# Kernel optimization log

Measured on AMD Instinct MI355X. Metric: run time of the kernel, lower is better.

## Reference

```python
import jax, jax.numpy as jnp
import numpy as np

B, N, U = 8, 2048, 256
BN_EPS = 1e-3  # keras BatchNormalization default epsilon
ADJ_DENSITY = 0.008  # ~16 neighbors per node on average


def setup_inputs() -> dict:
    key = jax.random.key(0)
    ks = jax.random.split(key, 16)
    s = 0.05  # weight scale ('random_normal' init is small-stddev in keras)
    x = jax.random.normal(ks[0], (B, N, U), jnp.float32)
    # sparse binary adjacency stored dense (per-sample SpMM pattern)
    adj = (jax.random.uniform(ks[1], (B, N, N)) < ADJ_DENSITY).astype(jnp.float32)
    nodal_mask = jnp.ones((B, N), jnp.float32)
    return {
        'x': x, 'adj': adj, 'nodal_mask': nodal_mask,
        'W_lin': jax.random.normal(ks[2], (U, U)) * s, 'b_lin': jnp.zeros((U,)),
        'Wq_mp': jax.random.normal(ks[3], (3, U, U)) * s, 'bq_mp': jnp.zeros((3, U)),
        'Wk_mp': jax.random.normal(ks[4], (3, U, U)) * s, 'bk_mp': jnp.zeros((3, U)),
        'Wv_mp': jax.random.normal(ks[5], (3, U, U)) * s, 'bv_mp': jnp.zeros((3, U)),
        'Wk_att': jax.random.normal(ks[6], (U, U)) * s,
        'Wv_att': jax.random.normal(ks[7], (U, U)) * s,
        'Wq_att': jax.random.normal(ks[8], (U, U)) * s,
        'Wo_att': jax.random.normal(ks[9], (U, U)) * s,
        'bn_gamma': jnp.ones((U,)), 'bn_beta': jnp.zeros((U,)),
        'bn_mean': jnp.zeros((U,)), 'bn_var': jnp.ones((U,)),
        'W_proj': jax.random.normal(ks[10], (U, U)) * s, 'b_proj': jnp.zeros((U,)),
        'W_res': jax.random.normal(ks[11], (U, U)) * s, 'b_res': jnp.zeros((U,)),
    }


def _dympn(x, adj, Ws, bs, mask):
    # 3 message-passing layers, each applied K_l=2 times (inference value)
    for i in range(3):
        for _ in range(2):
            xn = jnp.einsum('bmn,bnd->bmd', adj, x)  # batched SpMM (graph_conv mode)
            x = jax.nn.silu(jnp.einsum('bmd,de->bme', xn, Ws[i]) + bs[i])
    return x * mask[:, :, None]


def reference(x, adj, nodal_mask, W_lin, b_lin, Wq_mp, bq_mp, Wk_mp, bk_mp,
              Wv_mp, bv_mp, Wk_att, Wv_att, Wq_att, Wo_att,
              bn_gamma, bn_beta, bn_mean, bn_var, W_proj, b_proj, W_res, b_res):
    initial_x = x
    adj = jax.lax.stop_gradient(adj)
    h = jnp.einsum('bnd,de->bne', x, W_lin) + b_lin
    q = _dympn(h, adj, Wq_mp, bq_mp, nodal_mask)
    k = _dympn(h, adj, Wk_mp, bk_mp, nodal_mask)
    v = _dympn(h, adj, Wv_mp, bv_mp, nodal_mask)
    # linear attention
    m = nodal_mask[:, :, None]
    pk = jax.nn.silu(jnp.einsum('bnd,de->bne', k, Wk_att) * m)
    pv = jnp.einsum('bnd,de->bne', v, Wv_att) * m
    pq = jnp.einsum('bnd,de->bne', q, Wq_att)
    kv = jnp.einsum('bnd,bne->bde', pk, pv)       # [B,U,U]
    attn = jnp.einsum('bnd,bde->bne', pq, kv)
    attn = jnp.einsum('bnd,de->bne', attn, Wo_att)
    # batch norm (inference: moving stats) over last axis
    y = attn + initial_x
    y = bn_gamma * (y - bn_mean) * jax.lax.rsqrt(bn_var + BN_EPS) + bn_beta
    out = jax.nn.silu(jnp.einsum('bnd,de->bne', y, W_proj) + b_proj)
    out = out + jnp.einsum('bnd,de->bne', initial_x, W_res) + b_res
    out = out * nodal_mask[:, :, None]
    return out
```

## Files before the change

### kernel.cpp

```cpp
#include <hip/hip_runtime.h>
#include <stdint.h>

#define NB 8
#define NN 2048
#define NU 256
#define CAP 64
#define BNEPS 0.001f
#define GSTR ((size_t)(NN * NU + 256))

typedef __attribute__((ext_vector_type(8))) short short8;
typedef __attribute__((ext_vector_type(4))) float floatx4;
typedef unsigned short u16;
typedef unsigned int u32;

__device__ __forceinline__ float bf2f(u16 u) {
  union { u32 i; float f; } c; c.i = ((u32)u) << 16; return c.f;
}
__device__ __forceinline__ u16 f2bf(float f) {
  union { float f; u32 i; } c; c.f = f;
  return (u16)((c.i + 0x7fffu + ((c.i >> 16) & 1u)) >> 16);
}
__device__ __forceinline__ void splitbf(float a, u16& h, u16& l) {
  h = f2bf(a);
  l = f2bf(a - bf2f(h));
}

enum : unsigned {
  F_BIAS = 2u, F_SILU = 4u, F_MASKPRE = 8u, F_MASKPOST = 16u,
  F_ADDX = 32u, F_BN = 64u, F_ADDT = 128u, F_BPERMAT = 512u,
  F_TPLANES = 1024u, F_OUTHL = 2048u, F_GSTRIDE = 8192u
};

#define TP_MAT 524288
#define TP_LO  4194304
#define MSZ ((size_t)NN * NU)

struct WPtrs { const float* p[16]; };

__global__ __launch_bounds__(256) void prologue_k(
    WPtrs wp, u16* __restrict__ wdst,
    const float* __restrict__ x, u16* __restrict__ xdst, size_t xLo,
    const float* __restrict__ adj, int* __restrict__ cnt, int* __restrict__ idx,
    float* __restrict__ ga, float* __restrict__ gb)
{
  int bid = blockIdx.x;
  int tid = threadIdx.x;
  __shared__ int c0;
  if (bid < 512) {
    int gid = bid * 256 + tid;
    int mat = gid >> 13;
    int rem = gid & 8191;
    int kb = rem >> 10;
    int n = (rem >> 2) & 255;
    int slot = rem & 3;
    int qv = (slot - (n >> 1)) & 3;
    int k0 = kb * 32 + qv * 8;
    const float* W = wp.p[mat];
    u32 oh[4], ol[4];
#pragma unroll
    for (int t2 = 0; t2 < 4; t2++) {
      float f0 = W[(size_t)(k0 + 2 * t2) * 256 + n];
      float f1 = W[(size_t)(k0 + 2 * t2 + 1) * 256 + n];
      u16 h0, l0, h1, l1;
      splitbf(f0, h0, l0);
      splitbf(f1, h1, l1);
      oh[t2] = (u32)h0 | ((u32)h1 << 16);
      ol[t2] = (u32)l0 | ((u32)l1 << 16);
    }
    uint4 qh; qh.x = oh[0]; qh.y = oh[1]; qh.z = oh[2]; qh.w = oh[3];
    uint4 ql; ql.x = ol[0]; ql.y = ol[1]; ql.z = ol[2]; ql.w = ol[3];
    *(uint4*)(wdst + (size_t)gid * 8) = qh;
    *(uint4*)(wdst + 1048576 + (size_t)gid * 8) = ql;
  } else if (bid < 4608) {
    size_t i = ((size_t)(bid - 512) * 256 + tid) * 4;
    float4 v = *(const float4*)(x + i);
    u16 h0, l0, h1, l1, h2, l2, h3, l3;
    splitbf(v.x, h0, l0); splitbf(v.y, h1, l1);
    splitbf(v.z, h2, l2); splitbf(v.w, h3, l3);
    uint2 H; H.x = (u32)h0 | ((u32)h1 << 16); H.y = (u32)h2 | ((u32)h3 << 16);
    uint2 L; L.x = (u32)l0 | ((u32)l1 << 16); L.y = (u32)l2 | ((u32)l3 << 16);
    *(uint2*)(xdst + i) = H;
    *(uint2*)(xdst + xLo + i) = L;
  } else if (bid < 20992) {
    int row = bid - 4608;
    const float* base = adj + (size_t)row * NN;
    if (tid == 0) c0 = 0;
    __syncthreads();
#pragma unroll
    for (int j = 0; j < 8; j++) {
      int n = j * 256 + tid;
      if (base[n] != 0.f) {
        int p = atomicAdd(&c0, 1);
        if (p < CAP) idx[(size_t)row * CAP + p] = n;
      }
    }
    __syncthreads();
    int cc = (c0 < CAP ? c0 : CAP);
    for (int p = cc + tid; p < CAP; p += 256) idx[(size_t)row * CAP + p] = -1;
    if (tid == 0) cnt[row] = cc;
  } else {
    int g = bid - 20992;
    float* base = (g < 24 ? ga : gb) + (size_t)(g % 24) * GSTR;
    base[tid] = 0.f;
  }
}

template <unsigned F>
__device__ __forceinline__ void gemm_epi(
    floatx4 (&acc)[2][2], int b, int bm, int w, int m16, int q,
    const float* __restrict__ bias, const float* __restrict__ mask,
    const float* __restrict__ xf32,
    const float* __restrict__ gma, const float* __restrict__ bta,
    const float* __restrict__ bmu, const float* __restrict__ bvr,
    const float* __restrict__ addt, void* __restrict__ outp, size_t oLo)
{
#pragma unroll
  for (int mt = 0; mt < 2; mt++) {
    if (F & F_TPLANES) {
      u16* oh = (u16*)outp + (size_t)b * TP_MAT;
      u16* ol = oh + TP_LO;
      int gr0 = bm + mt * 16 + q * 4;
#pragma unroll
      for (int nt = 0; nt < 2; nt++) {
        int col = w * 32 + nt * 16 + m16;
        u16 hh[4], ll[4];
#pragma unroll
        for (int r = 0; r < 4; r++) {
          float t2 = acc[mt][nt][r];
          float mv = mask[b * NN + gr0 + r];
          if (F & F_MASKPRE) t2 *= mv;
          if (F & F_SILU) t2 = t2 / (1.f + __expf(-t2));
          if (F & F_MASKPOST) t2 *= mv;
          splitbf(t2, hh[r], ll[r]);
        }
        uint2 H2, L2v;
        H2.x = (u32)hh[0] | ((u32)hh[1] << 16);
        H2.y = (u32)hh[2] | ((u32)hh[3] << 16);
        L2v.x = (u32)ll[0] | ((u32)ll[1] << 16);
        L2v.y = (u32)ll[2] | ((u32)ll[3] << 16);
        *(uint2*)(oh + (size_t)col * 2048 + gr0) = H2;
        *(uint2*)(ol + (size_t)col * 2048 + gr0) = L2v;
      }
    } else {
#pragma unroll
      for (int r = 0; r < 4; r++) {
        int gr = bm + mt * 16 + q * 4 + r;
        float mval = 1.f;
        if (F & (F_MASKPRE | F_MASKPOST)) mval = mask[b * NN + gr];
#pragma unroll
        for (int nt = 0; nt < 2; nt++) {
          int col = w * 32 + nt * 16 + m16;
          float t2 = acc[mt][nt][r];
          if (F & F_BIAS) t2 += bias[col];
          if (F & F_MASKPRE) t2 *= mval;
          if (F & F_SILU) t2 = t2 / (1.f + __expf(-t2));
          if (F & F_ADDX) t2 += xf32[((size_t)b * NN + gr) * NU + col];
          if (F & F_BN) t2 = gma[col] * (t2 - bmu[col]) * rsqrtf(bvr[col] + BNEPS) + bta[col];
          if (F & F_ADDT) t2 += addt[((size_t)b * NN + gr) * NU + col];
          if (F & F_MASKPOST) t2 *= mval;
          size_t o;
          if (F & F_GSTRIDE) o = (size_t)b * GSTR + (size_t)gr * NU + col;
          else o = ((size_t)b * NN + gr) * NU + col;
          if (F & F_OUTHL) {
            u16 h0, l0;
            splitbf(t2, h0, l0);
            ((u16*)outp)[o] = h0;
            ((u16*)outp)[o + oLo] = l0;
          } else {
            ((float*)outp)[o] = t2;
          }
        }
      }
    }
  }
}

template <int NG, unsigned SF, unsigned F0, unsigned F1, unsigned F2, bool DK = false>
__global__ __launch_bounds__(512, 4) void gemm_k(
    const u16* __restrict__ A0, const u16* __restrict__ A1, const u16* __restrict__ A2,
    size_t aLo,
    const u16* __restrict__ W0, const u16* __restrict__ W1, const u16* __restrict__ W2,
    size_t wLo,
    const float* __restrict__ b0, const float* __restrict__ b1, const float* __restrict__ b2,
    const float* __restrict__ mask,
    const float* __restrict__ xf32,
    const float* __restrict__ gma, const float* __restrict__ bta,
    const float* __restrict__ bmu, const float* __restrict__ bvr,
    const float* __restrict__ addt,
    void* __restrict__ o0, void* __restrict__ o1, void* __restrict__ o2,
    size_t oLo,
    const float* __restrict__ gsrc,
    const float* __restrict__ sb0, const float* __restrict__ sb1, const float* __restrict__ sb2,
    const int* __restrict__ ncnt, const int* __restrict__ nidx)
{
  const int tid = threadIdx.x;
  const int id = blockIdx.x;
  const int xcd = id & 7;
  const int t = id >> 3;
  const int chain = (NG == 1) ? 0 : (t >> 6);
  const int xt = (NG == 1) ? t : (t & 63);
  const int b = xcd;
  const int bm = xt * 32;

  __shared__ alignas(16) u16 Ah[32 * 264];
  __shared__ alignas(16) u16 Al[32 * 264];

  const u16* Wsel = (chain == 0) ? W0 : (chain == 1 ? W1 : W2);
  if (F0 & F_BPERMAT) Wsel = W0 + (size_t)b * 65536;
  const u16* Whi = Wsel;
  const u16* Wlo = Whi + wLo;

  const int lane = tid & 63;
  const int w = tid >> 6;

  if constexpr (SF != 0u) {
    const float* __restrict__ gm = gsrc + (size_t)(chain * 8 + b) * GSTR + 256;
    const float* sb = (chain == 0) ? sb0 : (chain == 1 ? sb1 : sb2);
    const int c = lane * 4;
    float4 bb = *(const float4*)(sb + c);
    const int r0 = w * 4;
    const int* ips[4];
    float4 av[4];
    int rowids[4];
    int maxc = 0;
#pragma unroll
    for (int i = 0; i < 4; i++) {
      rowids[i] = b * NN + bm + r0 + i;
      int cn = ncnt[rowids[i]];
      maxc = cn > maxc ? cn : maxc;
      ips[i] = nidx + (size_t)rowids[i] * CAP;
      av[i].x = av[i].y = av[i].z = av[i].w = 0.f;
    }
    maxc = (maxc + 3) & ~3;
#pragma unroll 1
    for (int e = 0; e < maxc; e += 4) {
#pragma unroll
      for (int i = 0; i < 4; i++) {
        int4 i4 = *(const int4*)(ips[i] + e);
        float4 v0 = *(const float4*)(gm + (ptrdiff_t)i4.x * 256 + c);
        float4 v1 = *(const float4*)(gm + (ptrdiff_t)i4.y * 256 + c);
        float4 v2 = *(const float4*)(gm + (ptrdiff_t)i4.z * 256 + c);
        float4 v3 = *(const float4*)(gm + (ptrdiff_t)i4.w * 256 + c);
        av[i].x += v0.x + v1.x + v2.x + v3.x;
        av[i].y += v0.y + v1.y + v2.y + v3.y;
        av[i].z += v0.z + v1.z + v2.z + v3.z;
        av[i].w += v0.w + v1.w + v2.w + v3.w;
      }
    }
#pragma unroll
    for (int i = 0; i < 4; i++) {
      float ov[4] = {av[i].x + bb.x, av[i].y + bb.y, av[i].z + bb.z, av[i].w + bb.w};
      float mv = (SF & F_MASKPOST) ? mask[rowids[i]] : 1.f;
      u16 hh[4], ll[4];
#pragma unroll
      for (int j = 0; j < 4; j++) {
        float t2 = ov[j];
        if (SF & F_SILU) t2 = t2 / (1.f + __expf(-t2));
        if (SF & F_MASKPOST) t2 *= mv;
        splitbf(t2, hh[j], ll[j]);
      }
      uint2 H; H.x = (u32)hh[0] | ((u32)hh[1] << 16); H.y = (u32)hh[2] | ((u32)hh[3] << 16);
      uint2 L; L.x = (u32)ll[0] | ((u32)ll[1] << 16); L.y = (u32)ll[2] | ((u32)ll[3] << 16);
      *(uint2*)&Ah[(r0 + i) * 264 + c] = H;
      *(uint2*)&Al[(r0 + i) * 264 + c] = L;
    }
  } else {
    const u16* Abase = (chain == 0) ? A0 : (chain == 1 ? A1 : A2);
    const u16* Ahp = Abase + (size_t)b * MSZ;
    const u16* Alp = Ahp + aLo;
    {
      int s = tid;
      int r = s >> 4;
      int c = (s & 15) << 4;
      size_t ao = (size_t)(bm + r) * 256 + c;
      *(uint4*)&Ah[r * 264 + c] = *(const uint4*)(Ahp + ao);
      *(uint4*)&Ah[r * 264 + c + 8] = *(const uint4*)(Ahp + ao + 8);
      *(uint4*)&Al[r * 264 + c] = *(const uint4*)(Alp + ao);
      *(uint4*)&Al[r * 264 + c + 8] = *(const uint4*)(Alp + ao + 8);
    }
  }
  __syncthreads();

  const int m16 = lane & 15;
  const int q = lane >> 4;

  floatx4 acc[2][2];
#pragma unroll
  for (int i = 0; i < 2; i++)
#pragma unroll
    for (int j = 0; j < 2; j++) acc[i][j] = (floatx4){0.f, 0.f, 0.f, 0.f};

#pragma unroll
  for (int kk = 0; kk < 8; kk++) {
    short8 bh[2], bl2[2];
#pragma unroll
    for (int nt = 0; nt < 2; nt++) {
      int n = w * 32 + nt * 16 + m16;
      size_t off = (size_t)kk * 8192 + (size_t)n * 32 + (size_t)(((q + (n >> 1)) & 3) * 8);
      bh[nt] = *(const short8*)(Whi + off);
      bl2[nt] = *(const short8*)(Wlo + off);
    }
#pragma unroll
    for (int mt = 0; mt < 2; mt++) {
      int row = mt * 16 + m16;
      short8 ah = *(const short8*)&Ah[row * 264 + kk * 32 + q * 8];
      short8 al2 = *(const short8*)&Al[row * 264 + kk * 32 + q * 8];
#pragma unroll
      for (int nt = 0; nt < 2; nt++) {
        acc[mt][nt] = __builtin_amdgcn_mfma_f32_16x16x32_bf16(ah, bh[nt], acc[mt][nt], 0, 0, 0);
        acc[mt][nt] = __builtin_amdgcn_mfma_f32_16x16x32_bf16(al2, bh[nt], acc[mt][nt], 0, 0, 0);
        acc[mt][nt] = __builtin_amdgcn_mfma_f32_16x16x32_bf16(ah, bl2[nt], acc[mt][nt], 0, 0, 0);
      }
    }
  }

  if constexpr (DK) {
#pragma unroll
    for (int mt = 0; mt < 2; mt++)
#pragma unroll
      for (int nt = 0; nt < 2; nt++) {
        int col = w * 32 + nt * 16 + m16;
        float bp = b1[col];
#pragma unroll
        for (int r = 0; r < 4; r++) {
          float t2 = acc[mt][nt][r] + bp;
          acc[mt][nt][r] = t2 / (1.f + __expf(-t2));
        }
      }
    __syncthreads();
    {
      const u16* Ahp = A1 + (size_t)b * MSZ;
      const u16* Alp = Ahp + aLo;
      int s = tid;
      int r = s >> 4;
      int c = (s & 15) << 4;
      size_t ao = (size_t)(bm + r) * 256 + c;
      *(uint4*)&Ah[r * 264 + c] = *(const uint4*)(Ahp + ao);
      *(uint4*)&Ah[r * 264 + c + 8] = *(const uint4*)(Ahp + ao + 8);
      *(uint4*)&Al[r * 264 + c] = *(const uint4*)(Alp + ao);
      *(uint4*)&Al[r * 264 + c + 8] = *(const uint4*)(Alp + ao + 8);
    }
    __syncthreads();
    const u16* W1h = W1;
    const u16* W1l = W1 + wLo;
#pragma unroll
    for (int kk = 0; kk < 8; kk++) {
      short8 bh[2], bl2[2];
#pragma unroll
      for (int nt = 0; nt < 2; nt++) {
        int n = w * 32 + nt * 16 + m16;
        size_t off = (size_t)kk * 8192 + (size_t)n * 32 + (size_t)(((q + (n >> 1)) & 3) * 8);
        bh[nt] = *(const short8*)(W1h + off);
        bl2[nt] = *(const short8*)(W1l + off);
      }
#pragma unroll
      for (int mt = 0; mt < 2; mt++) {
        int row = mt * 16 + m16;
        short8 ah = *(const short8*)&Ah[row * 264 + kk * 32 + q * 8];
        short8 al2 = *(const short8*)&Al[row * 264 + kk * 32 + q * 8];
#pragma unroll
        for (int nt = 0; nt < 2; nt++) {
          acc[mt][nt] = __builtin_amdgcn_mfma_f32_16x16x32_bf16(ah, bh[nt], acc[mt][nt], 0, 0, 0);
          acc[mt][nt] = __builtin_amdgcn_mfma_f32_16x16x32_bf16(al2, bh[nt], acc[mt][nt], 0, 0, 0);
          acc[mt][nt] = __builtin_amdgcn_mfma_f32_16x16x32_bf16(ah, bl2[nt], acc[mt][nt], 0, 0, 0);
        }
      }
    }
  }

  if (NG == 1 || chain == 0)
    gemm_epi<F0>(acc, b, bm, w, m16, q, b0, mask, xf32, gma, bta, bmu, bvr, addt, o0, oLo);
  else if (chain == 1)
    gemm_epi<F1>(acc, b, bm, w, m16, q, b1, mask, xf32, gma, bta, bmu, bvr, addt, o1, oLo);
  else
    gemm_epi<F2>(acc, b, bm, w, m16, q, b2, mask, xf32, gma, bta, bmu, bvr, addt, o2, oLo);
}

__global__ __launch_bounds__(256, 2) void kv_k(
    const u16* __restrict__ pkT, const u16* __restrict__ pvT, float* __restrict__ part)
{
  int et = blockIdx.x * 128;
  int dt = blockIdx.y * 128;
  int z = blockIdx.z;
  int b = z & 7;
  int p = z >> 3;
  int tid = threadIdx.x;
  int lane = tid & 63, w = tid >> 6;
  int m16 = lane & 15, q = lane >> 4;

  const u16* pkh = pkT + (size_t)b * TP_MAT;
  const u16* pkl = pkh + TP_LO;
  const u16* pvh = pvT + (size_t)b * TP_MAT;
  const u16* pvl = pvh + TP_LO;

  int d_base = dt + (w >> 1) * 64 + m16;
  int e_base = et + (w & 1) * 64 + m16;

  floatx4 acc[4][4];
#pragma unroll
  for (int i = 0; i < 4; i++)
#pragma unroll
    for (int j = 0; j < 4; j++) acc[i][j] = (floatx4){0.f, 0.f, 0.f, 0.f};

#pragma unroll
  for (int kt = 0; kt < 8; kt++) {
    int kc = p * 256 + kt * 32 + q * 8;
    short8 ah[4], al[4], bh[4], bl[4];
#pragma unroll
    for (int mt = 0; mt < 4; mt++) {
      size_t o = (size_t)(d_base + mt * 16) * 2048 + kc;
      ah[mt] = *(const short8*)(pkh + o);
      al[mt] = *(const short8*)(pkl + o);
    }
#pragma unroll
    for (int nt = 0; nt < 4; nt++) {
      size_t o = (size_t)(e_base + nt * 16) * 2048 + kc;
      bh[nt] = *(const short8*)(pvh + o);
      bl[nt] = *(const short8*)(pvl + o);
    }
#pragma unroll
    for (int mt = 0; mt < 4; mt++)
#pragma unroll
      for (int nt = 0; nt < 4; nt++) {
        acc[mt][nt] = __builtin_amdgcn_mfma_f32_16x16x32_bf16(ah[mt], bh[nt], acc[mt][nt], 0, 0, 0);
        acc[mt][nt] = __builtin_amdgcn_mfma_f32_16x16x32_bf16(al[mt], bh[nt], acc[mt][nt], 0, 0, 0);
        acc[mt][nt] = __builtin_amdgcn_mfma_f32_16x16x32_bf16(ah[mt], bl[nt], acc[mt][nt], 0, 0, 0);
      }
  }

#pragma unroll
  for (int mt = 0; mt < 4; mt++)
#pragma unroll
    for (int r = 0; r < 4; r++) {
      int d = dt + (w >> 1) * 64 + mt * 16 + q * 4 + r;
#pragma unroll
      for (int nt = 0; nt < 4; nt++) {
        int e = et + (w & 1) * 64 + nt * 16 + m16;
        part[(size_t)z * 65536 + (size_t)d * 256 + e] = acc[mt][nt][r];
      }
    }
}

__global__ __launch_bounds__(256) void kv_conv_k(const float* __restrict__ part, u16* __restrict__ dst)
{
  int gid = blockIdx.x * 256 + threadIdx.x;
  int b = gid >> 13;
  int rem = gid & 8191;
  int kb = rem >> 10;
  int e = (rem >> 2) & 255;
  int slot = rem & 3;
  int qv = (slot - (e >> 1)) & 3;
  int d0 = kb * 32 + qv * 8;
  const float* src = part + (size_t)b * 65536 + (size_t)d0 * 256 + e;
  u32 oh[4], ol[4];
#pragma unroll
  for (int t2 = 0; t2 < 4; t2++) {
    float s0 = 0.f, s1 = 0.f;
#pragma unroll
    for (int pp = 0; pp < 8; pp++) {
      const float* sp = src + (size_t)pp * 524288 + t2 * 512;
      s0 += sp[0];
      s1 += sp[256];
    }
    u16 h0, l0, h1, l1;
    splitbf(s0, h0, l0);
    splitbf(s1, h1, l1);
    oh[t2] = (u32)h0 | ((u32)h1 << 16);
    ol[t2] = (u32)l0 | ((u32)l1 << 16);
  }
  uint4 qh; qh.x = oh[0]; qh.y = oh[1]; qh.z = oh[2]; qh.w = oh[3];
  uint4 ql; ql.x = ol[0]; ql.y = ol[1]; ql.z = ol[2]; ql.w = ol[3];
  *(uint4*)(dst + (size_t)gid * 8) = qh;
  *(uint4*)(dst + 524288 + (size_t)gid * 8) = ql;
}

extern "C" void kernel_launch(void* const* d_in, const int* in_sizes, int n_in,
                              void* d_out, int out_size, void* d_ws, size_t ws_size,
                              hipStream_t stream)
{
  const float* x = (const float*)d_in[0];
  const float* adj = (const float*)d_in[1];
  const float* mask = (const float*)d_in[2];
  const float* W_lin = (const float*)d_in[3];
  const float* b_lin = (const float*)d_in[4];
  const float* Wq_mp = (const float*)d_in[5];
  const float* bq_mp = (const float*)d_in[6];
  const float* Wk_mp = (const float*)d_in[7];
  const float* bk_mp = (const float*)d_in[8];
  const float* Wv_mp = (const float*)d_in[9];
  const float* bv_mp = (const float*)d_in[10];
  const float* Wk_att = (const float*)d_in[11];
  const float* Wv_att = (const float*)d_in[12];
  const float* Wq_att = (const float*)d_in[13];
  const float* Wo_att = (const float*)d_in[14];
  const float* bn_gamma = (const float*)d_in[15];
  const float* bn_beta = (const float*)d_in[16];
  const float* bn_mean = (const float*)d_in[17];
  const float* bn_var = (const float*)d_in[18];
  const float* W_proj = (const float*)d_in[19];
  const float* b_proj = (const float*)d_in[20];
  const float* W_res = (const float*)d_in[21];
  const float* b_res = (const float*)d_in[22];

  char* ws = (char*)d_ws;
  int* CNT    = (int*)(ws + 0);
  int* IDX    = (int*)(ws + (1ull << 20));
  u16* WSZ    = (u16*)(ws + (5ull << 20));
  u16* KVS    = (u16*)(ws + (9ull << 20));
  float* KVP  = (float*)(ws + (11ull << 20));
  u16* XHL    = (u16*)(ws + (27ull << 20));
  u16* HHL    = (u16*)(ws + (43ull << 20));
  float* GA   = (float*)(ws + (59ull << 20));
  float* GB   = (float*)(ws + (110ull << 20));
  u16* PKT    = (u16*)(ws + (161ull << 20));
  u16* PVT    = (u16*)(ws + (177ull << 20));
  u16* ATT    = (u16*)(ws + (193ull << 20));
  u16* YHL    = (u16*)(ws + (209ull << 20));
  u16* PQHL   = (u16*)(ws + (225ull << 20));

  const size_t WLO = 1048576;
  const size_t KLO = 524288;
  const size_t A8  = 8 * MSZ;
  const unsigned FG = F_GSTRIDE;

  WPtrs wp;
  wp.p[0] = W_lin;
  wp.p[1] = Wq_mp; wp.p[2] = Wq_mp + 65536; wp.p[3] = Wq_mp + 131072;
  wp.p[4] = Wk_mp; wp.p[5] = Wk_mp + 65536; wp.p[6] = Wk_mp + 131072;
  wp.p[7] = Wv_mp; wp.p[8] = Wv_mp + 65536; wp.p[9] = Wv_mp + 131072;
  wp.p[10] = Wk_att; wp.p[11] = Wv_att; wp.p[12] = Wq_att; wp.p[13] = Wo_att;
  wp.p[14] = W_proj; wp.p[15] = W_res;
  prologue_k<<<21040, 256, 0, stream>>>(wp, WSZ, x, XHL, A8, adj, CNT, IDX, GA, GB);

  gemm_k<1, 0u, F_BIAS | F_OUTHL, 0u, 0u><<<512, 512, 0, stream>>>(
      XHL, XHL, XHL, A8, WSZ, WSZ, WSZ, WLO,
      b_lin, nullptr, nullptr, mask, nullptr,
      bn_gamma, bn_beta, bn_mean, bn_var, nullptr,
      HHL, nullptr, nullptr, A8,
      nullptr, nullptr, nullptr, nullptr, CNT, IDX);

  gemm_k<3, 0u, FG, FG, FG><<<1536, 512, 0, stream>>>(
      HHL, HHL, HHL, A8,
      WSZ + (size_t)1 * 65536, WSZ + (size_t)4 * 65536, WSZ + (size_t)7 * 65536, WLO,
      nullptr, nullptr, nullptr, mask, nullptr,
      bn_gamma, bn_beta, bn_mean, bn_var, nullptr,
      GA + 256, GA + 8 * GSTR + 256, GA + 16 * GSTR + 256, 0,
      nullptr, nullptr, nullptr, nullptr, CNT, IDX);

  for (int s = 1; s < 6; s++) {
    int iw = s >> 1;
    int ib = (s - 1) >> 1;
    float* Gin = (s & 1) ? GA : GB;
    float* Gout = (s & 1) ? GB : GA;
    gemm_k<3, F_BIAS | F_SILU, FG, FG, FG><<<1536, 512, 0, stream>>>(
        nullptr, nullptr, nullptr, 0,
        WSZ + (size_t)(1 + iw) * 65536, WSZ + (size_t)(4 + iw) * 65536,
        WSZ + (size_t)(7 + iw) * 65536, WLO,
        nullptr, nullptr, nullptr, mask, nullptr,
        bn_gamma, bn_beta, bn_mean, bn_var, nullptr,
        Gout + 256, Gout + 8 * GSTR + 256, Gout + 16 * GSTR + 256, 0,
        Gin, bq_mp + ib * 256, bk_mp + ib * 256, bv_mp + ib * 256, CNT, IDX);
  }

  gemm_k<3, F_BIAS | F_SILU | F_MASKPOST,
         F_OUTHL, F_SILU | F_MASKPRE | F_TPLANES, F_MASKPOST | F_TPLANES>
      <<<1536, 512, 0, stream>>>(
      nullptr, nullptr, nullptr, 0,
      WSZ + (size_t)12 * 65536, WSZ + (size_t)10 * 65536, WSZ + (size_t)11 * 65536, WLO,
      nullptr, nullptr, nullptr, mask, nullptr,
      bn_gamma, bn_beta, bn_mean, bn_var, nullptr,
      PQHL, PKT, PVT, A8,
      GB, bq_mp + 512, bk_mp + 512, bv_mp + 512, CNT, IDX);

  kv_k<<<dim3(2, 2, 64), 256, 0, stream>>>(PKT, PVT, KVP);
  kv_conv_k<<<256, 256, 0, stream>>>(KVP, KVS);

  gemm_k<1, 0u, F_BPERMAT | F_OUTHL, 0u, 0u><<<512, 512, 0, stream>>>(
      PQHL, PQHL, PQHL, A8, KVS, KVS, KVS, KLO,
      nullptr, nullptr, nullptr, mask, nullptr,
      bn_gamma, bn_beta, bn_mean, bn_var, nullptr,
      ATT, nullptr, nullptr, A8,
      nullptr, nullptr, nullptr, nullptr, CNT, IDX);

  gemm_k<1, 0u, F_ADDX | F_BN | F_OUTHL, 0u, 0u><<<512, 512, 0, stream>>>(
      ATT, ATT, ATT, A8,
      WSZ + (size_t)13 * 65536, nullptr, nullptr, WLO,
      nullptr, nullptr, nullptr, mask, x,
      bn_gamma, bn_beta, bn_mean, bn_var, nullptr,
      YHL, nullptr, nullptr, A8,
      nullptr, nullptr, nullptr, nullptr, CNT, IDX);

  gemm_k<1, 0u, F_BIAS | F_MASKPOST, 0u, 0u, true><<<512, 512, 0, stream>>>(
      YHL, XHL, YHL, A8,
      WSZ + (size_t)14 * 65536, WSZ + (size_t)15 * 65536, nullptr, WLO,
      b_res, b_proj, nullptr, mask, nullptr,
      bn_gamma, bn_beta, bn_mean, bn_var, nullptr,
      d_out, nullptr, nullptr, 0,
      nullptr, nullptr, nullptr, nullptr, CNT, IDX);

  (void)in_sizes; (void)n_in; (void)out_size; (void)ws_size;
}
```

Measured before the change: 754.4 us.

## Stage GSTRIDE epilogue through LDS with nontemporal stores, per-row gather bounds

```diff
diff --git a/kernel.cpp b/kernel.cpp
--- a/kernel.cpp
+++ b/kernel.cpp
@@ -158,9 +158,7 @@
           if (F & F_BN) t2 = gma[col] * (t2 - bmu[col]) * rsqrtf(bvr[col] + BNEPS) + bta[col];
           if (F & F_ADDT) t2 += addt[((size_t)b * NN + gr) * NU + col];
           if (F & F_MASKPOST) t2 *= mval;
-          size_t o;
-          if (F & F_GSTRIDE) o = (size_t)b * GSTR + (size_t)gr * NU + col;
-          else o = ((size_t)b * NN + gr) * NU + col;
+          size_t o = ((size_t)b * NN + gr) * NU + col;
           if (F & F_OUTHL) {
             u16 h0, l0;
             splitbf(t2, h0, l0);
@@ -176,7 +174,7 @@
 }
 
 template <int NG, unsigned SF, unsigned F0, unsigned F1, unsigned F2, bool DK = false>
-__global__ __launch_bounds__(512, 4) void gemm_k(
+__global__ __launch_bounds__(512, 8) void gemm_k(
     const u16* __restrict__ A0, const u16* __restrict__ A1, const u16* __restrict__ A2,
     size_t aLo,
     const u16* __restrict__ W0, const u16* __restrict__ W1, const u16* __restrict__ W2,
@@ -202,8 +200,9 @@
   const int b = xcd;
   const int bm = xt * 32;
 
-  __shared__ alignas(16) u16 Ah[32 * 264];
-  __shared__ alignas(16) u16 Al[32 * 264];
+  __shared__ alignas(16) u16 AB[2 * 32 * 264];
+  u16* const Ah = AB;
+  u16* const Al = AB + 32 * 264;
 
   const u16* Wsel = (chain == 0) ? W0 : (chain == 1 ? W1 : W2);
   if (F0 & F_BPERMAT) Wsel = W0 + (size_t)b * 65536;
@@ -219,32 +218,42 @@
     const int c = lane * 4;
     float4 bb = *(const float4*)(sb + c);
     const int r0 = w * 4;
+    int cnts[4];
     const int* ips[4];
     float4 av[4];
     int rowids[4];
-    int maxc = 0;
 #pragma unroll
     for (int i = 0; i < 4; i++) {
       rowids[i] = b * NN + bm + r0 + i;
-      int cn = ncnt[rowids[i]];
-      maxc = cn > maxc ? cn : maxc;
+      cnts[i] = ncnt[rowids[i]];
       ips[i] = nidx + (size_t)rowids[i] * CAP;
       av[i].x = av[i].y = av[i].z = av[i].w = 0.f;
     }
-    maxc = (maxc + 3) & ~3;
-#pragma unroll 1
-    for (int e = 0; e < maxc; e += 4) {
+    int maxc = cnts[0];
+    maxc = cnts[1] > maxc ? cnts[1] : maxc;
+    maxc = cnts[2] > maxc ? cnts[2] : maxc;
+    maxc = cnts[3] > maxc ? cnts[3] : maxc;
+    for (int e = 0; e + 4 <= maxc; e += 4) {
 #pragma unroll
       for (int i = 0; i < 4; i++) {
-        int4 i4 = *(const int4*)(ips[i] + e);
-        float4 v0 = *(const float4*)(gm + (ptrdiff_t)i4.x * 256 + c);
-        float4 v1 = *(const float4*)(gm + (ptrdiff_t)i4.y * 256 + c);
-        float4 v2 = *(const float4*)(gm + (ptrdiff_t)i4.z * 256 + c);
-        float4 v3 = *(const float4*)(gm + (ptrdiff_t)i4.w * 256 + c);
-        av[i].x += v0.x + v1.x + v2.x + v3.x;
-        av[i].y += v0.y + v1.y + v2.y + v3.y;
-        av[i].z += v0.z + v1.z + v2.z + v3.z;
-        av[i].w += v0.w + v1.w + v2.w + v3.w;
+        if (e + 4 <= cnts[i]) {
+          int4 i4 = *(const int4*)(ips[i] + e);
+          float4 v0 = *(const float4*)(gm + ((size_t)i4.x << 8) + c);
+          float4 v1 = *(const float4*)(gm + ((size_t)i4.y << 8) + c);
+          float4 v2 = *(const float4*)(gm + ((size_t)i4.z << 8) + c);
+          float4 v3 = *(const float4*)(gm + ((size_t)i4.w << 8) + c);
+          av[i].x += v0.x + v1.x + v2.x + v3.x;
+          av[i].y += v0.y + v1.y + v2.y + v3.y;
+          av[i].z += v0.z + v1.z + v2.z + v3.z;
+          av[i].w += v0.w + v1.w + v2.w + v3.w;
+        }
+      }
+    }
+#pragma unroll
+    for (int i = 0; i < 4; i++) {
+      for (int e = cnts[i] & ~3; e < cnts[i]; e++) {
+        float4 v = *(const float4*)(gm + ((size_t)ips[i][e] << 8) + c);
+        av[i].x += v.x; av[i].y += v.y; av[i].z += v.z; av[i].w += v.w;
       }
     }
 #pragma unroll
@@ -368,12 +377,36 @@
     }
   }
 
-  if (NG == 1 || chain == 0)
+  if constexpr ((F0 & F_GSTRIDE) != 0u) {
+    void* op = (NG == 1 || chain == 0) ? o0 : (chain == 1 ? o1 : o2);
+    __syncthreads();
+    float* Cf = (float*)AB;
+#pragma unroll
+    for (int mt = 0; mt < 2; mt++)
+#pragma unroll
+      for (int nt = 0; nt < 2; nt++) {
+        int col = w * 32 + nt * 16 + m16;
+#pragma unroll
+        for (int r = 0; r < 4; r++)
+          Cf[(mt * 16 + q * 4 + r) * 256 + col] = acc[mt][nt][r];
+      }
+    __syncthreads();
+    int r2 = tid >> 4;
+    int cs = (tid & 15) * 16;
+    float* dst = (float*)op + (size_t)b * GSTR + (size_t)(bm + r2) * 256 + cs;
+    const float* srcp = Cf + r2 * 256 + cs;
+#pragma unroll
+    for (int j = 0; j < 4; j++) {
+      floatx4 v4 = *(const floatx4*)(srcp + j * 4);
+      __builtin_nontemporal_store(v4, (floatx4*)(dst + j * 4));
+    }
+  } else if (NG == 1 || chain == 0) {
     gemm_epi<F0>(acc, b, bm, w, m16, q, b0, mask, xf32, gma, bta, bmu, bvr, addt, o0, oLo);
-  else if (chain == 1)
+  } else if (chain == 1) {
     gemm_epi<F1>(acc, b, bm, w, m16, q, b1, mask, xf32, gma, bta, bmu, bvr, addt, o1, oLo);
-  else
+  } else {
     gemm_epi<F2>(acc, b, bm, w, m16, q, b2, mask, xf32, gma, bta, bmu, bvr, addt, o2, oLo);
+  }
 }
 
 __global__ __launch_bounds__(256, 2) void kv_k(
```

New measurement: 991.3 us. +31.4%, slower.

## Stream SpMM neighbor gathers through per-wave LDS ring via global_load_lds

Applied to the files above, without the earlier changes.

```diff
diff --git a/kernel.cpp b/kernel.cpp
--- a/kernel.cpp
+++ b/kernel.cpp
@@ -8,6 +8,9 @@
 #define BNEPS 0.001f
 #define GSTR ((size_t)(NN * NU + 256))
 
+#define REG16 2256
+#define REGB  4512
+
 typedef __attribute__((ext_vector_type(8))) short short8;
 typedef __attribute__((ext_vector_type(4))) float floatx4;
 typedef unsigned short u16;
@@ -24,6 +27,20 @@
   h = f2bf(a);
   l = f2bf(a - bf2f(h));
 }
+
+__device__ __forceinline__ void gld_lds16(const float* g, void* l) {
+  __builtin_amdgcn_global_load_lds(
+      (const __attribute__((address_space(1))) u32*)g,
+      (__attribute__((address_space(3))) u32*)l, 16, 0, 0);
+}
+__device__ __forceinline__ void gld_lds4(const int* g, void* l) {
+  __builtin_amdgcn_global_load_lds(
+      (const __attribute__((address_space(1))) u32*)g,
+      (__attribute__((address_space(3))) u32*)l, 4, 0, 0);
+}
+
+#define WAITV0 { asm volatile("s_waitcnt vmcnt(0)" ::: "memory"); __builtin_amdgcn_sched_barrier(0); }
+#define WAITV2 { asm volatile("s_waitcnt vmcnt(2)" ::: "memory"); __builtin_amdgcn_sched_barrier(0); }
 
 enum : unsigned {
   F_BIAS = 2u, F_SILU = 4u, F_MASKPRE = 8u, F_MASKPOST = 16u,
@@ -176,7 +193,7 @@
 }
 
 template <int NG, unsigned SF, unsigned F0, unsigned F1, unsigned F2, bool DK = false>
-__global__ __launch_bounds__(512, 4) void gemm_k(
+__global__ __launch_bounds__(512, 8) void gemm_k(
     const u16* __restrict__ A0, const u16* __restrict__ A1, const u16* __restrict__ A2,
     size_t aLo,
     const u16* __restrict__ W0, const u16* __restrict__ W1, const u16* __restrict__ W2,
@@ -202,8 +219,7 @@
   const int b = xcd;
   const int bm = xt * 32;
 
-  __shared__ alignas(16) u16 Ah[32 * 264];
-  __shared__ alignas(16) u16 Al[32 * 264];
+  __shared__ alignas(16) u16 AB[8 * REG16];
 
   const u16* Wsel = (chain == 0) ? W0 : (chain == 1 ? W1 : W2);
   if (F0 & F_BPERMAT) Wsel = W0 + (size_t)b * 65536;
@@ -216,40 +232,82 @@
   if constexpr (SF != 0u) {
     const float* __restrict__ gm = gsrc + (size_t)(chain * 8 + b) * GSTR + 256;
     const float* sb = (chain == 0) ? sb0 : (chain == 1 ? sb1 : sb2);
-    const int c = lane * 4;
-    float4 bb = *(const float4*)(sb + c);
-    const int r0 = w * 4;
+    const int c4 = lane * 4;
+    float4 bb = *(const float4*)(sb + c4);
+    char* const wreg = (char*)AB + w * REGB;
+    char* const ring = wreg;
+    int* const idxl = (int*)(wreg + 4096);
+
+    float4 av4[4];
+    int cnts[4], rowids[4];
     const int* ips[4];
-    float4 av[4];
-    int rowids[4];
-    int maxc = 0;
 #pragma unroll
     for (int i = 0; i < 4; i++) {
-      rowids[i] = b * NN + bm + r0 + i;
-      int cn = ncnt[rowids[i]];
-      maxc = cn > maxc ? cn : maxc;
+      rowids[i] = b * NN + bm + w * 4 + i;
+      cnts[i] = ncnt[rowids[i]];
       ips[i] = nidx + (size_t)rowids[i] * CAP;
-      av[i].x = av[i].y = av[i].z = av[i].w = 0.f;
-    }
-    maxc = (maxc + 3) & ~3;
+    }
+
 #pragma unroll 1
-    for (int e = 0; e < maxc; e += 4) {
-#pragma unroll
-      for (int i = 0; i < 4; i++) {
-        int4 i4 = *(const int4*)(ips[i] + e);
-        float4 v0 = *(const float4*)(gm + (ptrdiff_t)i4.x * 256 + c);
-        float4 v1 = *(const float4*)(gm + (ptrdiff_t)i4.y * 256 + c);
-        float4 v2 = *(const float4*)(gm + (ptrdiff_t)i4.z * 256 + c);
-        float4 v3 = *(const float4*)(gm + (ptrdiff_t)i4.w * 256 + c);
-        av[i].x += v0.x + v1.x + v2.x + v3.x;
-        av[i].y += v0.y + v1.y + v2.y + v3.y;
-        av[i].z += v0.z + v1.z + v2.z + v3.z;
-        av[i].w += v0.w + v1.w + v2.w + v3.w;
-      }
-    }
-#pragma unroll
     for (int i = 0; i < 4; i++) {
-      float ov[4] = {av[i].x + bb.x, av[i].y + bb.y, av[i].z + bb.z, av[i].w + bb.w};
+      const int cnt = cnts[i];
+      float4 a; a.x = a.y = a.z = a.w = 0.f;
+      gld_lds4(ips[i] + lane, idxl);
+      WAITV0;
+      const int cnt4 = cnt & ~3;
+      if (cnt4 > 0) {
+        int4 i0 = *(const int4*)idxl;
+        gld_lds16(gm + ((size_t)i0.x << 8) + c4, ring);
+        gld_lds16(gm + ((size_t)i0.y << 8) + c4, ring + 1024);
+        gld_lds16(gm + ((size_t)i0.z << 8) + c4, ring + 2048);
+        gld_lds16(gm + ((size_t)i0.w << 8) + c4, ring + 3072);
+#pragma unroll 1
+        for (int e = 4; e < cnt4; e += 4) {
+          int4 nx = *(const int4*)(idxl + e);
+          WAITV2;
+          float4 v0 = *(const float4*)(ring + lane * 16);
+          float4 v1 = *(const float4*)(ring + 1024 + lane * 16);
+          float4 tt;
+          tt.x = v0.x + v1.x; tt.y = v0.y + v1.y;
+          tt.z = v0.z + v1.z; tt.w = v0.w + v1.w;
+          gld_lds16(gm + ((size_t)nx.x << 8) + c4, ring);
+          gld_lds16(gm + ((size_t)nx.y << 8) + c4, ring + 1024);
+          WAITV2;
+          float4 v2 = *(const float4*)(ring + 2048 + lane * 16);
+          float4 v3 = *(const float4*)(ring + 3072 + lane * 16);
+          tt.x = (tt.x + v2.x) + v3.x; tt.y = (tt.y + v2.y) + v3.y;
+          tt.z = (tt.z + v2.z) + v3.z; tt.w = (tt.w + v2.w) + v3.w;
+          a.x += tt.x; a.y += tt.y; a.z += tt.z; a.w += tt.w;
+          gld_lds16(gm + ((size_t)nx.z << 8) + c4, ring + 2048);
+          gld_lds16(gm + ((size_t)nx.w << 8) + c4, ring + 3072);
+        }
+        WAITV2;
+        float4 v0 = *(const float4*)(ring + lane * 16);
+        float4 v1 = *(const float4*)(ring + 1024 + lane * 16);
+        float4 tt;
+        tt.x = v0.x + v1.x; tt.y = v0.y + v1.y;
+        tt.z = v0.z + v1.z; tt.w = v0.w + v1.w;
+        WAITV0;
+        float4 v2 = *(const float4*)(ring + 2048 + lane * 16);
+        float4 v3 = *(const float4*)(ring + 3072 + lane * 16);
+        tt.x = (tt.x + v2.x) + v3.x; tt.y = (tt.y + v2.y) + v3.y;
+        tt.z = (tt.z + v2.z) + v3.z; tt.w = (tt.w + v2.w) + v3.w;
+        a.x += tt.x; a.y += tt.y; a.z += tt.z; a.w += tt.w;
+      }
+#pragma unroll 1
+      for (int e = cnt4; e < cnt; e++) {
+        int n = idxl[e];
+        gld_lds16(gm + ((size_t)n << 8) + c4, ring);
+        WAITV0;
+        float4 v = *(const float4*)(ring + lane * 16);
+        a.x += v.x; a.y += v.y; a.z += v.z; a.w += v.w;
+      }
+      av4[i] = a;
+    }
+
+#pragma unroll
+    for (int i = 0; i < 4; i++) {
+      float ov[4] = {av4[i].x + bb.x, av4[i].y + bb.y, av4[i].z + bb.z, av4[i].w + bb.w};
       float mv = (SF & F_MASKPOST) ? mask[rowids[i]] : 1.f;
       u16 hh[4], ll[4];
 #pragma unroll
@@ -261,8 +319,8 @@
       }
       uint2 H; H.x = (u32)hh[0] | ((u32)hh[1] << 16); H.y = (u32)hh[2] | ((u32)hh[3] << 16);
       uint2 L; L.x = (u32)ll[0] | ((u32)ll[1] << 16); L.y = (u32)ll[2] | ((u32)ll[3] << 16);
-      *(uint2*)&Ah[(r0 + i) * 264 + c] = H;
-      *(uint2*)&Al[(r0 + i) * 264 + c] = L;
+      *(uint2*)&AB[w * REG16 + i * 264 + c4] = H;
+      *(uint2*)&AB[w * REG16 + 1056 + i * 264 + c4] = L;
     }
   } else {
     const u16* Abase = (chain == 0) ? A0 : (chain == 1 ? A1 : A2);
@@ -273,10 +331,11 @@
       int r = s >> 4;
       int c = (s & 15) << 4;
       size_t ao = (size_t)(bm + r) * 256 + c;
-      *(uint4*)&Ah[r * 264 + c] = *(const uint4*)(Ahp + ao);
-      *(uint4*)&Ah[r * 264 + c + 8] = *(const uint4*)(Ahp + ao + 8);
-      *(uint4*)&Al[r * 264 + c] = *(const uint4*)(Alp + ao);
-      *(uint4*)&Al[r * 264 + c + 8] = *(const uint4*)(Alp + ao + 8);
+      int base = (r >> 2) * REG16 + (r & 3) * 264 + c;
+      *(uint4*)&AB[base] = *(const uint4*)(Ahp + ao);
+      *(uint4*)&AB[base + 8] = *(const uint4*)(Ahp + ao + 8);
+      *(uint4*)&AB[base + 1056] = *(const uint4*)(Alp + ao);
+      *(uint4*)&AB[base + 1056 + 8] = *(const uint4*)(Alp + ao + 8);
     }
   }
   __syncthreads();
@@ -303,8 +362,9 @@
 #pragma unroll
     for (int mt = 0; mt < 2; mt++) {
       int row = mt * 16 + m16;
-      short8 ah = *(const short8*)&Ah[row * 264 + kk * 32 + q * 8];
-      short8 al2 = *(const short8*)&Al[row * 264 + kk * 32 + q * 8];
+      int abase = (row >> 2) * REG16 + (row & 3) * 264 + kk * 32 + q * 8;
+      short8 ah = *(const short8*)&AB[abase];
+      short8 al2 = *(const short8*)&AB[abase + 1056];
 #pragma unroll
       for (int nt = 0; nt < 2; nt++) {
         acc[mt][nt] = __builtin_amdgcn_mfma_f32_16x16x32_bf16(ah, bh[nt], acc[mt][nt], 0, 0, 0);
@@ -335,10 +395,11 @@
       int r = s >> 4;
       int c = (s & 15) << 4;
       size_t ao = (size_t)(bm + r) * 256 + c;
-      *(uint4*)&Ah[r * 264 + c] = *(const uint4*)(Ahp + ao);
-      *(uint4*)&Ah[r * 264 + c + 8] = *(const uint4*)(Ahp + ao + 8);
-      *(uint4*)&Al[r * 264 + c] = *(const uint4*)(Alp + ao);
-      *(uint4*)&Al[r * 264 + c + 8] = *(const uint4*)(Alp + ao + 8);
+      int base = (r >> 2) * REG16 + (r & 3) * 264 + c;
+      *(uint4*)&AB[base] = *(const uint4*)(Ahp + ao);
+      *(uint4*)&AB[base + 8] = *(const uint4*)(Ahp + ao + 8);
+      *(uint4*)&AB[base + 1056] = *(const uint4*)(Alp + ao);
+      *(uint4*)&AB[base + 1056 + 8] = *(const uint4*)(Alp + ao + 8);
     }
     __syncthreads();
     const u16* W1h = W1;
@@ -356,8 +417,9 @@
 #pragma unroll
       for (int mt = 0; mt < 2; mt++) {
         int row = mt * 16 + m16;
-        short8 ah = *(const short8*)&Ah[row * 264 + kk * 32 + q * 8];
-        short8 al2 = *(const short8*)&Al[row * 264 + kk * 32 + q * 8];
+        int abase = (row >> 2) * REG16 + (row & 3) * 264 + kk * 32 + q * 8;
+        short8 ah = *(const short8*)&AB[abase];
+        short8 al2 = *(const short8*)&AB[abase + 1056];
 #pragma unroll
         for (int nt = 0; nt < 2; nt++) {
           acc[mt][nt] = __builtin_amdgcn_mfma_f32_16x16x32_bf16(ah, bh[nt], acc[mt][nt], 0, 0, 0);
```

After: 839.5 us. +11.3%, slower.
